# Optimization experiments

Hardware: AMD Instinct MI355X
Metric: run time of the kernel (lower is better)

Reference implementation:

```python
import jax, jax.numpy as jnp
import numpy as np

T = 0.2  # temperature (init default)
EPS = 1e-12  # torch F.normalize eps


def setup_inputs() -> dict:
    key = jax.random.key(0)
    k1, k2 = jax.random.split(key, 2)
    b, in_c, out_c = 8192, 128, 128
    anchor_features = jax.random.normal(k1, (b, in_c), dtype=jnp.float32)
    W = jax.random.normal(k2, (in_c, out_c), dtype=jnp.float32) * (1.0 / np.sqrt(in_c))
    bias = jnp.zeros((out_c,), dtype=jnp.float32)
    return {"anchor_features": anchor_features, "W": W, "bias": bias}


def reference(anchor_features, W, bias):
    # MappingLayer: linear projection + L2 normalize, then pairwise cosine sims.
    z = anchor_features @ W + bias                                  # [b, d]
    z = z / jnp.maximum(jnp.linalg.norm(z, axis=-1, keepdims=True), EPS)
    sim = (z @ z.T) / T                                             # [b, b]
    b = sim.shape[0]
    idx = jnp.arange(b)
    j0 = (idx + b // 2) % b                                         # positive pair index
    # Fused symmetric exp matrix: E[i,j] = exp(sim[i,j] + sim[j,i])
    E = jnp.exp(sim + sim.T)                                        # [b, b]
    top = E[idx, j0]                                                # exp(s_ij0 + s_j0i)
    bottom = jnp.sum(E, axis=1) - E[idx, idx]                       # sum over j != i
    loss = -jnp.sum(jnp.log(top / bottom)) / (b - 1)
    return loss
```

## Files before the change

kernel.cpp:

```cpp
#include <hip/hip_runtime.h>
#include <stdint.h>

typedef short bf16x8 __attribute__((ext_vector_type(8)));
typedef float f32x4 __attribute__((ext_vector_type(4)));

#define NROWS 8192
#define DIM   128
#define ZSCALE 3.7982824f
#define LN2F  0.6931471805599453f


__device__ __forceinline__ unsigned short f32_to_bf16_bits(float x) {
  union { float f; uint32_t u; } v; v.f = x;
  uint32_t r = v.u + 0x7FFFu + ((v.u >> 16) & 1u);
  return (unsigned short)(r >> 16);
}

__global__ __launch_bounds__(256) void k_wprep(const float* __restrict__ W,
                                               unsigned short* __restrict__ Wtf,
                                               float* __restrict__ sumexp,
                                               float* __restrict__ topacc) {
  const int idx = blockIdx.x * 256 + threadIdx.x;
  if (idx < 2048) {
    const int l = idx & 63, chunk = idx >> 6;
    const int tj = chunk >> 2, ks = chunk & 3, g = l >> 4, q = l & 15;
    const float* wp = W + (size_t)(ks * 32 + g * 8) * DIM + tj * 16 + q;
    bf16x8 o;
#pragma unroll
    for (int e = 0; e < 8; ++e) o[e] = (short)f32_to_bf16_bits(wp[(size_t)e * DIM]);
    *(bf16x8*)(Wtf + (size_t)idx * 8) = o;
  }
  if (idx < NROWS) sumexp[idx] = 0.f;
  if (idx == 0) topacc[0] = 0.f;
}

__global__ __launch_bounds__(256) void k_proj_norm(
    const float* __restrict__ anchor, const unsigned short* __restrict__ Wtf,
    const float* __restrict__ bias, unsigned short* __restrict__ zf) {
  __shared__ float part[4][16][132];
  const int t = threadIdx.x;
  const int wv = t >> 6, l = t & 63, g = l >> 4, q = l & 15;
  const int rb = blockIdx.x * 16;

  const float* ap = anchor + (size_t)(rb + q) * DIM + wv * 32 + g * 8;
  const f32x4 a0 = *(const f32x4*)ap, a1 = *(const f32x4*)(ap + 4);
  bf16x8 a;
#pragma unroll
  for (int e = 0; e < 4; ++e) {
    a[e] = (short)f32_to_bf16_bits(a0[e]);
    a[4 + e] = (short)f32_to_bf16_bits(a1[e]);
  }

  f32x4 acc[8];
#pragma unroll
  for (int tj = 0; tj < 8; ++tj) acc[tj] = (f32x4){0.f, 0.f, 0.f, 0.f};
#pragma unroll
  for (int tj = 0; tj < 8; ++tj) {
    const bf16x8 b = *(const bf16x8*)(Wtf + (size_t)((tj * 4 + wv) * 64 + l) * 8);
    acc[tj] = __builtin_amdgcn_mfma_f32_16x16x32_bf16(a, b, acc[tj], 0, 0, 0);
  }

#pragma unroll
  for (int tj = 0; tj < 8; ++tj)
#pragma unroll
    for (int r = 0; r < 4; ++r) part[wv][4 * g + r][tj * 16 + q] = acc[tj][r];
  __syncthreads();

  const int row = t >> 4, c = t & 15;
  float v[8];
#pragma unroll
  for (int e = 0; e < 8; ++e) v[e] = bias[c * 8 + e];
#pragma unroll
  for (int s = 0; s < 4; ++s) {
    const f32x4 p0 = *(const f32x4*)&part[s][row][c * 8];
    const f32x4 p1 = *(const f32x4*)&part[s][row][c * 8 + 4];
#pragma unroll
    for (int e = 0; e < 4; ++e) {
      v[e] += p0[e];
      v[4 + e] += p1[e];
    }
  }
  float ss = 0.f;
#pragma unroll
  for (int e = 0; e < 8; ++e) ss += v[e] * v[e];
#pragma unroll
  for (int m = 1; m < 16; m <<= 1) ss += __shfl_xor(ss, m, 64);
  const float inv = ZSCALE / fmaxf(sqrtf(ss), 1e-12f);

  bf16x8 o;
#pragma unroll
  for (int e = 0; e < 8; ++e) o[e] = (short)f32_to_bf16_bits(v[e] * inv);
  const int ks = c >> 2, gg = c & 3;
  *(bf16x8*)(zf + (size_t)(((blockIdx.x * 4 + ks) * 64) + gg * 16 + row) * 8) = o;
}

__global__ __launch_bounds__(256) void k_simloss(
    const unsigned short* __restrict__ zf, float* __restrict__ sumexp,
    float* __restrict__ topacc) {
  const int t = threadIdx.x;
  const int wv = t >> 6, l = t & 63, g = l >> 4, q = l & 15;
  const int igrp = (int)blockIdx.x >> 5, jbi = (int)blockIdx.x & 31;
  const int r0 = igrp * 256 + wv * 64;
  const int cb = jbi * 256;
  const int posr = (r0 + 4096) & 8191;

  bf16x8 afr[4][4];
#pragma unroll
  for (int ti = 0; ti < 4; ++ti)
#pragma unroll
    for (int ks = 0; ks < 4; ++ks)
      afr[ti][ks] = *(const bf16x8*)(
          zf + (size_t)((((r0 >> 4) + ti) * 4 + ks) * 512 + l * 8));

  float sums[4][4];
#pragma unroll
  for (int ti = 0; ti < 4; ++ti)
#pragma unroll
    for (int r = 0; r < 4; ++r) sums[ti][r] = 0.f;
  float topv = 0.f;

  bool qeq[4];
#pragma unroll
  for (int r = 0; r < 4; ++r) qeq[r] = (q == 4 * g + r);

  auto LOADB = [&](bf16x8 b[4], int c0) {
    const int bcol = c0 >> 4;
#pragma unroll
    for (int ks = 0; ks < 4; ++ks)
      b[ks] = *(const bf16x8*)(zf + (size_t)((bcol * 4 + ks) * 512 + l * 8));
  };
  auto COMPUTE = [&](const bf16x8 b[4], int c0) {
    f32x4 acc[4];
#pragma unroll
    for (int ti = 0; ti < 4; ++ti) acc[ti] = (f32x4){0.f, 0.f, 0.f, 0.f};
#pragma unroll
    for (int ti = 0; ti < 4; ++ti)
#pragma unroll
      for (int ks = 0; ks < 4; ++ks)
        acc[ti] = __builtin_amdgcn_mfma_f32_16x16x32_bf16(afr[ti][ks], b[ks],
                                                          acc[ti], 0, 0, 0);
    const int dgo = c0 - r0, pso = c0 - posr;
    const int dgti = ((unsigned)dgo < 64u) ? (dgo >> 4) : -1;
    const int psti = ((unsigned)pso < 64u) ? (pso >> 4) : -1;
#pragma unroll
    for (int ti = 0; ti < 4; ++ti) {
#pragma unroll
      for (int r = 0; r < 4; ++r) {
        const float d = acc[ti][r];
        float e = __builtin_amdgcn_exp2f(d);
        if (ti == dgti && qeq[r]) e = 0.f;
        if (ti == psti && qeq[r]) topv += d;
        sums[ti][r] += e;
      }
    }
  };

  bf16x8 bA[4], bB[4];
  LOADB(bA, cb);
#pragma unroll
  for (int p = 0; p < 8; ++p) {
    LOADB(bB, cb + p * 32 + 16);
    COMPUTE(bA, cb + p * 32);
    if (p < 7) LOADB(bA, cb + p * 32 + 32);
    COMPUTE(bB, cb + p * 32 + 16);
  }

#pragma unroll
  for (int ti = 0; ti < 4; ++ti)
#pragma unroll
    for (int r = 0; r < 4; ++r) {
#pragma unroll
      for (int m = 1; m < 16; m <<= 1)
        sums[ti][r] += __shfl_xor(sums[ti][r], m, 64);
    }
  if (q == 0) {
#pragma unroll
    for (int ti = 0; ti < 4; ++ti)
#pragma unroll
      for (int r = 0; r < 4; ++r)
        atomicAdd(&sumexp[r0 + ti * 16 + 4 * g + r], sums[ti][r]);
  }

  if ((posr & ~255) == cb) {
#pragma unroll
    for (int m = 1; m < 64; m <<= 1) topv += __shfl_xor(topv, m, 64);
    if (l == 0) atomicAdd(topacc, topv);
  }
}

__global__ __launch_bounds__(256) void k_final(const float* __restrict__ sumexp,
                                               const float* __restrict__ topacc,
                                               float* __restrict__ out) {
  __shared__ float red[4];
  const int t = threadIdx.x;
  float s = 0.f;
  for (int r = t; r < NROWS; r += 256) s += logf(sumexp[r]);
#pragma unroll
  for (int m = 1; m < 64; m <<= 1) s += __shfl_xor(s, m, 64);
  if ((t & 63) == 0) red[t >> 6] = s;
  __syncthreads();
  if (t == 0) {
    const float S1 = red[0] + red[1] + red[2] + red[3];
    out[0] = (S1 - LN2F * topacc[0]) * (1.0f / (float)(NROWS - 1));
  }
}

extern "C" void kernel_launch(void* const* d_in, const int* in_sizes, int n_in,
                              void* d_out, int out_size, void* d_ws, size_t ws_size,
                              hipStream_t stream) {
  const float* anchor = (const float*)d_in[0];
  const float* W = (const float*)d_in[1];
  const float* bias = (const float*)d_in[2];
  float* out = (float*)d_out;

  char* ws = (char*)d_ws;
  unsigned short* zf = (unsigned short*)ws;
  float* sumexp = (float*)(ws + (size_t)2 * 1024 * 1024);
  float* topacc = (float*)(ws + (size_t)2 * 1024 * 1024 + 32768);
  unsigned short* Wtf = (unsigned short*)(ws + (size_t)2 * 1024 * 1024 + 36864);

  k_wprep<<<dim3(64), dim3(256), 0, stream>>>(W, Wtf, sumexp, topacc);
  k_proj_norm<<<dim3(NROWS / 16), dim3(256), 0, stream>>>(anchor, Wtf, bias, zf);
  k_simloss<<<dim3(32 * 32), dim3(256), 0, stream>>>(zf, sumexp, topacc);
  k_final<<<dim3(1), dim3(256), 0, stream>>>(sumexp, topacc, out);
}
```

Measured before the change: 51.13 us.

## Exploit symmetry of sim matrix to compute only upper-triangular block tiles

Because the fused exp matrix is symmetric, the similarity kernel now launches only upper-triangular 256x256 block tiles (528 instead of 1024). Off-diagonal tiles add their exp values to both the row sums and, through per-column reductions and atomics, the column sums. The positive-pair term is counted once and doubled. The projection kernel also changes to a single wave per 16 rows doing the full K loop, so the cross-wave shared-memory reduction goes away, and the final reduction uses 1024 threads with log2. This roughly halves the MFMA and exp work, at the cost of extra column atomics and a triangular index decode.

Result: no change. 52.09 us (+1.9%).

```diff
diff --git a/kernel.cpp b/kernel.cpp
--- a/kernel.cpp
+++ b/kernel.cpp
@@ -34,64 +34,174 @@
   if (idx == 0) topacc[0] = 0.f;
 }
 
-__global__ __launch_bounds__(256) void k_proj_norm(
+__global__ __launch_bounds__(64) void k_proj_norm(
     const float* __restrict__ anchor, const unsigned short* __restrict__ Wtf,
     const float* __restrict__ bias, unsigned short* __restrict__ zf) {
-  __shared__ float part[4][16][132];
-  const int t = threadIdx.x;
-  const int wv = t >> 6, l = t & 63, g = l >> 4, q = l & 15;
+  __shared__ __align__(16) float part[16][132];
+  const int l = threadIdx.x, g = l >> 4, q = l & 15;
   const int rb = blockIdx.x * 16;
 
-  const float* ap = anchor + (size_t)(rb + q) * DIM + wv * 32 + g * 8;
-  const f32x4 a0 = *(const f32x4*)ap, a1 = *(const f32x4*)(ap + 4);
-  bf16x8 a;
-#pragma unroll
-  for (int e = 0; e < 4; ++e) {
-    a[e] = (short)f32_to_bf16_bits(a0[e]);
-    a[4 + e] = (short)f32_to_bf16_bits(a1[e]);
+  bf16x8 a[4];
+#pragma unroll
+  for (int ks = 0; ks < 4; ++ks) {
+    const float* ap = anchor + (size_t)(rb + q) * DIM + ks * 32 + g * 8;
+    const f32x4 a0 = *(const f32x4*)ap, a1 = *(const f32x4*)(ap + 4);
+#pragma unroll
+    for (int e = 0; e < 4; ++e) {
+      a[ks][e] = (short)f32_to_bf16_bits(a0[e]);
+      a[ks][4 + e] = (short)f32_to_bf16_bits(a1[e]);
+    }
   }
 
   f32x4 acc[8];
 #pragma unroll
   for (int tj = 0; tj < 8; ++tj) acc[tj] = (f32x4){0.f, 0.f, 0.f, 0.f};
 #pragma unroll
+  for (int tj = 0; tj < 8; ++tj)
+#pragma unroll
+    for (int ks = 0; ks < 4; ++ks) {
+      const bf16x8 b = *(const bf16x8*)(Wtf + (size_t)((tj * 4 + ks) * 64 + l) * 8);
+      acc[tj] = __builtin_amdgcn_mfma_f32_16x16x32_bf16(a[ks], b, acc[tj], 0, 0, 0);
+    }
+
+  float sumsq[4] = {0.f, 0.f, 0.f, 0.f};
+#pragma unroll
   for (int tj = 0; tj < 8; ++tj) {
-    const bf16x8 b = *(const bf16x8*)(Wtf + (size_t)((tj * 4 + wv) * 64 + l) * 8);
-    acc[tj] = __builtin_amdgcn_mfma_f32_16x16x32_bf16(a, b, acc[tj], 0, 0, 0);
-  }
+    const float bv = bias[tj * 16 + q];
+#pragma unroll
+    for (int r = 0; r < 4; ++r) {
+      acc[tj][r] += bv;
+      sumsq[r] += acc[tj][r] * acc[tj][r];
+    }
+  }
+#pragma unroll
+  for (int r = 0; r < 4; ++r) {
+#pragma unroll
+    for (int m = 1; m < 16; m <<= 1) sumsq[r] += __shfl_xor(sumsq[r], m, 64);
+  }
+  float inv[4];
+#pragma unroll
+  for (int r = 0; r < 4; ++r) inv[r] = ZSCALE / fmaxf(sqrtf(sumsq[r]), 1e-12f);
 
 #pragma unroll
   for (int tj = 0; tj < 8; ++tj)
 #pragma unroll
-    for (int r = 0; r < 4; ++r) part[wv][4 * g + r][tj * 16 + q] = acc[tj][r];
-  __syncthreads();
-
-  const int row = t >> 4, c = t & 15;
-  float v[8];
-#pragma unroll
-  for (int e = 0; e < 8; ++e) v[e] = bias[c * 8 + e];
-#pragma unroll
-  for (int s = 0; s < 4; ++s) {
-    const f32x4 p0 = *(const f32x4*)&part[s][row][c * 8];
-    const f32x4 p1 = *(const f32x4*)&part[s][row][c * 8 + 4];
+    for (int r = 0; r < 4; ++r) part[4 * g + r][tj * 16 + q] = acc[tj][r] * inv[r];
+
+#pragma unroll
+  for (int ks = 0; ks < 4; ++ks) {
+    const f32x4 p0 = *(const f32x4*)&part[q][ks * 32 + g * 8];
+    const f32x4 p1 = *(const f32x4*)&part[q][ks * 32 + g * 8 + 4];
+    bf16x8 o;
 #pragma unroll
     for (int e = 0; e < 4; ++e) {
-      v[e] += p0[e];
-      v[4 + e] += p1[e];
-    }
-  }
-  float ss = 0.f;
-#pragma unroll
-  for (int e = 0; e < 8; ++e) ss += v[e] * v[e];
-#pragma unroll
-  for (int m = 1; m < 16; m <<= 1) ss += __shfl_xor(ss, m, 64);
-  const float inv = ZSCALE / fmaxf(sqrtf(ss), 1e-12f);
-
-  bf16x8 o;
-#pragma unroll
-  for (int e = 0; e < 8; ++e) o[e] = (short)f32_to_bf16_bits(v[e] * inv);
-  const int ks = c >> 2, gg = c & 3;
-  *(bf16x8*)(zf + (size_t)(((blockIdx.x * 4 + ks) * 64) + gg * 16 + row) * 8) = o;
+      o[e] = (short)f32_to_bf16_bits(p0[e]);
+      o[4 + e] = (short)f32_to_bf16_bits(p1[e]);
+    }
+    *(bf16x8*)(zf + (size_t)((blockIdx.x * 4 + ks) * 64 + l) * 8) = o;
+  }
+}
+
+template <int MODE>
+__device__ __forceinline__ void simloss_body(
+    const unsigned short* __restrict__ zf, float* __restrict__ sumexp,
+    float* __restrict__ topacc, const int r0, const int cb, const int l,
+    const int g, const int q) {
+  bf16x8 afr[4][4];
+#pragma unroll
+  for (int ti = 0; ti < 4; ++ti)
+#pragma unroll
+    for (int ks = 0; ks < 4; ++ks)
+      afr[ti][ks] = *(const bf16x8*)(
+          zf + (size_t)((((r0 >> 4) + ti) * 4 + ks) * 512 + l * 8));
+
+  float sums[4][4];
+#pragma unroll
+  for (int ti = 0; ti < 4; ++ti)
+#pragma unroll
+    for (int r = 0; r < 4; ++r) sums[ti][r] = 0.f;
+  float topv = 0.f;
+  const int posr = r0 + 4096;
+
+  bool qeq[4];
+#pragma unroll
+  for (int r = 0; r < 4; ++r) qeq[r] = (q == 4 * g + r);
+
+  auto LOADB = [&](bf16x8 b[4], int c0) {
+    const int bcol = c0 >> 4;
+#pragma unroll
+    for (int ks = 0; ks < 4; ++ks)
+      b[ks] = *(const bf16x8*)(zf + (size_t)((bcol * 4 + ks) * 512 + l * 8));
+  };
+  auto COMPUTE = [&](const bf16x8 b[4], int c0) {
+    f32x4 acc[4];
+#pragma unroll
+    for (int ti = 0; ti < 4; ++ti) acc[ti] = (f32x4){0.f, 0.f, 0.f, 0.f};
+#pragma unroll
+    for (int ti = 0; ti < 4; ++ti)
+#pragma unroll
+      for (int ks = 0; ks < 4; ++ks)
+        acc[ti] = __builtin_amdgcn_mfma_f32_16x16x32_bf16(afr[ti][ks], b[ks],
+                                                          acc[ti], 0, 0, 0);
+    int dgti = -1, psti = -1;
+    if (MODE == 0) {
+      const int dgo = c0 - r0;
+      dgti = ((unsigned)dgo < 64u) ? (dgo >> 4) : -1;
+    }
+    if (MODE == 2) {
+      const int pso = c0 - posr;
+      psti = ((unsigned)pso < 64u) ? (pso >> 4) : -1;
+    }
+    float cs = 0.f;
+#pragma unroll
+    for (int ti = 0; ti < 4; ++ti)
+#pragma unroll
+      for (int r = 0; r < 4; ++r) {
+        const float d = acc[ti][r];
+        float e = __builtin_amdgcn_exp2f(d);
+        if (MODE == 0 && ti == dgti && qeq[r]) e = 0.f;
+        if (MODE == 2 && ti == psti && qeq[r]) topv += d;
+        sums[ti][r] += e;
+        if (MODE != 0) cs += e;
+      }
+    if (MODE != 0) {
+      cs += __shfl_xor(cs, 16, 64);
+      cs += __shfl_xor(cs, 32, 64);
+      if (l < 16) atomicAdd(&sumexp[c0 + q], cs);
+    }
+  };
+
+  bf16x8 bA[4], bB[4];
+  LOADB(bA, cb);
+#pragma unroll
+  for (int p = 0; p < 8; ++p) {
+    LOADB(bB, cb + p * 32 + 16);
+    COMPUTE(bA, cb + p * 32);
+    if (p < 7) LOADB(bA, cb + p * 32 + 32);
+    COMPUTE(bB, cb + p * 32 + 16);
+  }
+
+#pragma unroll
+  for (int ti = 0; ti < 4; ++ti)
+#pragma unroll
+    for (int r = 0; r < 4; ++r) {
+#pragma unroll
+      for (int m = 1; m < 16; m <<= 1)
+        sums[ti][r] += __shfl_xor(sums[ti][r], m, 64);
+    }
+  if (q == 0) {
+#pragma unroll
+    for (int ti = 0; ti < 4; ++ti)
+#pragma unroll
+      for (int r = 0; r < 4; ++r)
+        atomicAdd(&sumexp[r0 + ti * 16 + 4 * g + r], sums[ti][r]);
+  }
+
+  if (MODE == 2) {
+#pragma unroll
+    for (int m = 1; m < 64; m <<= 1) topv += __shfl_xor(topv, m, 64);
+    if (l == 0) atomicAdd(topacc, 2.f * topv);
+  }
 }
 
 __global__ __launch_bounds__(256) void k_simloss(
@@ -99,109 +209,32 @@
     float* __restrict__ topacc) {
   const int t = threadIdx.x;
   const int wv = t >> 6, l = t & 63, g = l >> 4, q = l & 15;
-  const int igrp = (int)blockIdx.x >> 5, jbi = (int)blockIdx.x & 31;
+  int rem = (int)blockIdx.x, igrp = 0;
+  while (rem >= 32 - igrp) { rem -= 32 - igrp; ++igrp; }
+  const int jbi = igrp + rem;
   const int r0 = igrp * 256 + wv * 64;
   const int cb = jbi * 256;
-  const int posr = (r0 + 4096) & 8191;
-
-  bf16x8 afr[4][4];
-#pragma unroll
-  for (int ti = 0; ti < 4; ++ti)
-#pragma unroll
-    for (int ks = 0; ks < 4; ++ks)
-      afr[ti][ks] = *(const bf16x8*)(
-          zf + (size_t)((((r0 >> 4) + ti) * 4 + ks) * 512 + l * 8));
-
-  float sums[4][4];
-#pragma unroll
-  for (int ti = 0; ti < 4; ++ti)
-#pragma unroll
-    for (int r = 0; r < 4; ++r) sums[ti][r] = 0.f;
-  float topv = 0.f;
-
-  bool qeq[4];
-#pragma unroll
-  for (int r = 0; r < 4; ++r) qeq[r] = (q == 4 * g + r);
-
-  auto LOADB = [&](bf16x8 b[4], int c0) {
-    const int bcol = c0 >> 4;
-#pragma unroll
-    for (int ks = 0; ks < 4; ++ks)
-      b[ks] = *(const bf16x8*)(zf + (size_t)((bcol * 4 + ks) * 512 + l * 8));
-  };
-  auto COMPUTE = [&](const bf16x8 b[4], int c0) {
-    f32x4 acc[4];
-#pragma unroll
-    for (int ti = 0; ti < 4; ++ti) acc[ti] = (f32x4){0.f, 0.f, 0.f, 0.f};
-#pragma unroll
-    for (int ti = 0; ti < 4; ++ti)
-#pragma unroll
-      for (int ks = 0; ks < 4; ++ks)
-        acc[ti] = __builtin_amdgcn_mfma_f32_16x16x32_bf16(afr[ti][ks], b[ks],
-                                                          acc[ti], 0, 0, 0);
-    const int dgo = c0 - r0, pso = c0 - posr;
-    const int dgti = ((unsigned)dgo < 64u) ? (dgo >> 4) : -1;
-    const int psti = ((unsigned)pso < 64u) ? (pso >> 4) : -1;
-#pragma unroll
-    for (int ti = 0; ti < 4; ++ti) {
-#pragma unroll
-      for (int r = 0; r < 4; ++r) {
-        const float d = acc[ti][r];
-        float e = __builtin_amdgcn_exp2f(d);
-        if (ti == dgti && qeq[r]) e = 0.f;
-        if (ti == psti && qeq[r]) topv += d;
-        sums[ti][r] += e;
-      }
-    }
-  };
-
-  bf16x8 bA[4], bB[4];
-  LOADB(bA, cb);
-#pragma unroll
-  for (int p = 0; p < 8; ++p) {
-    LOADB(bB, cb + p * 32 + 16);
-    COMPUTE(bA, cb + p * 32);
-    if (p < 7) LOADB(bA, cb + p * 32 + 32);
-    COMPUTE(bB, cb + p * 32 + 16);
-  }
-
-#pragma unroll
-  for (int ti = 0; ti < 4; ++ti)
-#pragma unroll
-    for (int r = 0; r < 4; ++r) {
-#pragma unroll
-      for (int m = 1; m < 16; m <<= 1)
-        sums[ti][r] += __shfl_xor(sums[ti][r], m, 64);
-    }
-  if (q == 0) {
-#pragma unroll
-    for (int ti = 0; ti < 4; ++ti)
-#pragma unroll
-      for (int r = 0; r < 4; ++r)
-        atomicAdd(&sumexp[r0 + ti * 16 + 4 * g + r], sums[ti][r]);
-  }
-
-  if ((posr & ~255) == cb) {
-#pragma unroll
-    for (int m = 1; m < 64; m <<= 1) topv += __shfl_xor(topv, m, 64);
-    if (l == 0) atomicAdd(topacc, topv);
-  }
-}
-
-__global__ __launch_bounds__(256) void k_final(const float* __restrict__ sumexp,
-                                               const float* __restrict__ topacc,
-                                               float* __restrict__ out) {
-  __shared__ float red[4];
+  if (igrp == jbi)           simloss_body<0>(zf, sumexp, topacc, r0, cb, l, g, q);
+  else if (jbi == igrp + 16) simloss_body<2>(zf, sumexp, topacc, r0, cb, l, g, q);
+  else                       simloss_body<1>(zf, sumexp, topacc, r0, cb, l, g, q);
+}
+
+__global__ __launch_bounds__(1024) void k_final(const float* __restrict__ sumexp,
+                                                const float* __restrict__ topacc,
+                                                float* __restrict__ out) {
+  __shared__ float red[16];
   const int t = threadIdx.x;
   float s = 0.f;
-  for (int r = t; r < NROWS; r += 256) s += logf(sumexp[r]);
+  for (int r = t; r < NROWS; r += 1024) s += __log2f(sumexp[r]);
 #pragma unroll
   for (int m = 1; m < 64; m <<= 1) s += __shfl_xor(s, m, 64);
   if ((t & 63) == 0) red[t >> 6] = s;
   __syncthreads();
   if (t == 0) {
-    const float S1 = red[0] + red[1] + red[2] + red[3];
-    out[0] = (S1 - LN2F * topacc[0]) * (1.0f / (float)(NROWS - 1));
+    float S1 = 0.f;
+#pragma unroll
+    for (int i = 0; i < 16; ++i) S1 += red[i];
+    out[0] = LN2F * (S1 - topacc[0]) * (1.0f / (float)(NROWS - 1));
   }
 }
 
@@ -220,7 +253,7 @@
   unsigned short* Wtf = (unsigned short*)(ws + (size_t)2 * 1024 * 1024 + 36864);
 
   k_wprep<<<dim3(64), dim3(256), 0, stream>>>(W, Wtf, sumexp, topacc);
-  k_proj_norm<<<dim3(NROWS / 16), dim3(256), 0, stream>>>(anchor, Wtf, bias, zf);
-  k_simloss<<<dim3(32 * 32), dim3(256), 0, stream>>>(zf, sumexp, topacc);
-  k_final<<<dim3(1), dim3(256), 0, stream>>>(sumexp, topacc, out);
-}
+  k_proj_norm<<<dim3(NROWS / 16), dim3(64), 0, stream>>>(anchor, Wtf, bias, zf);
+  k_simloss<<<dim3(528), dim3(256), 0, stream>>>(zf, sumexp, topacc);
+  k_final<<<dim3(1), dim3(1024), 0, stream>>>(sumexp, topacc, out);
+}
```

## Stage B tiles into LDS via async global_load_lds double buffering

Applied to the files above, without the earlier changes.

Before, each of the four waves loaded the shared column block of z straight from global memory into registers. Now the block stages each 64-column chunk into a double-buffered 32 KB LDS area using direct global-to-LDS loads, so each tile is fetched once per block and all waves read it from LDS. This adds a barrier per chunk and more LDS use, which may lower occupancy. The final reduction kernel also moves to 1024 threads and uses log2 with a single ln2 scale at the end.

Result: faster. 42.09 us (-17.7%).

```diff
diff --git a/kernel.cpp b/kernel.cpp
--- a/kernel.cpp
+++ b/kernel.cpp
@@ -15,6 +15,11 @@
   uint32_t r = v.u + 0x7FFFu + ((v.u >> 16) & 1u);
   return (unsigned short)(r >> 16);
 }
+
+#define GLOAD_LDS16(gsrc, ldst)                                      \
+  __builtin_amdgcn_global_load_lds(                                  \
+      (const __attribute__((address_space(1))) unsigned int*)(gsrc), \
+      (__attribute__((address_space(3))) unsigned int*)(ldst), 16, 0, 0)
 
 __global__ __launch_bounds__(256) void k_wprep(const float* __restrict__ W,
                                                unsigned short* __restrict__ Wtf,
@@ -97,6 +102,7 @@
 __global__ __launch_bounds__(256) void k_simloss(
     const unsigned short* __restrict__ zf, float* __restrict__ sumexp,
     float* __restrict__ topacc) {
+  __shared__ __align__(16) unsigned short lz[2 * 8192];
   const int t = threadIdx.x;
   const int wv = t >> 6, l = t & 63, g = l >> 4, q = l & 15;
   const int igrp = (int)blockIdx.x >> 5, jbi = (int)blockIdx.x & 31;
@@ -119,51 +125,57 @@
     for (int r = 0; r < 4; ++r) sums[ti][r] = 0.f;
   float topv = 0.f;
 
-  bool qeq[4];
-#pragma unroll
-  for (int r = 0; r < 4; ++r) qeq[r] = (q == 4 * g + r);
-
-  auto LOADB = [&](bf16x8 b[4], int c0) {
-    const int bcol = c0 >> 4;
-#pragma unroll
-    for (int ks = 0; ks < 4; ++ks)
-      b[ks] = *(const bf16x8*)(zf + (size_t)((bcol * 4 + ks) * 512 + l * 8));
-  };
-  auto COMPUTE = [&](const bf16x8 b[4], int c0) {
-    f32x4 acc[4];
-#pragma unroll
-    for (int ti = 0; ti < 4; ++ti) acc[ti] = (f32x4){0.f, 0.f, 0.f, 0.f};
-#pragma unroll
-    for (int ti = 0; ti < 4; ++ti)
+#define STAGE(bufsel, c_)                                                    \
+  _Pragma("unroll") for (int it = 0; it < 4; ++it) {                         \
+    const char* src = (const char*)zf +                                      \
+                      ((size_t)(jbi * 64 + (c_)*16) << 10) +                 \
+                      ((it * 256 + t) << 4);                                 \
+    GLOAD_LDS16(src, (char*)lz + (bufsel)*16384 + it * 4096 + wv * 1024);    \
+  }
+
+  STAGE(0, 0);
+  __syncthreads();
+
+#pragma unroll
+  for (int c = 0; c < 4; ++c) {
+    if (c < 3) STAGE((c + 1) & 1, c + 1);
+
+    const unsigned short* buf = lz + (c & 1) * 8192;
+#pragma unroll
+    for (int jt = 0; jt < 4; ++jt) {
+      bf16x8 bfr[4];
 #pragma unroll
       for (int ks = 0; ks < 4; ++ks)
-        acc[ti] = __builtin_amdgcn_mfma_f32_16x16x32_bf16(afr[ti][ks], b[ks],
-                                                          acc[ti], 0, 0, 0);
-    const int dgo = c0 - r0, pso = c0 - posr;
-    const int dgti = ((unsigned)dgo < 64u) ? (dgo >> 4) : -1;
-    const int psti = ((unsigned)pso < 64u) ? (pso >> 4) : -1;
-#pragma unroll
-    for (int ti = 0; ti < 4; ++ti) {
-#pragma unroll
-      for (int r = 0; r < 4; ++r) {
-        const float d = acc[ti][r];
-        float e = __builtin_amdgcn_exp2f(d);
-        if (ti == dgti && qeq[r]) e = 0.f;
-        if (ti == psti && qeq[r]) topv += d;
-        sums[ti][r] += e;
-      }
+        bfr[ks] = *(const bf16x8*)(buf + (size_t)((jt * 4 + ks) * 64 + l) * 8);
+
+      f32x4 acc[4];
+#pragma unroll
+      for (int ti = 0; ti < 4; ++ti) acc[ti] = (f32x4){0.f, 0.f, 0.f, 0.f};
+#pragma unroll
+      for (int ti = 0; ti < 4; ++ti)
+#pragma unroll
+        for (int ks = 0; ks < 4; ++ks)
+          acc[ti] = __builtin_amdgcn_mfma_f32_16x16x32_bf16(afr[ti][ks], bfr[ks],
+                                                            acc[ti], 0, 0, 0);
+
+      const int c0 = cb + c * 64 + jt * 16;
+      const int dgo = c0 - r0, pso = c0 - posr;
+      const int dgti = ((unsigned)dgo < 64u) ? (dgo >> 4) : -1;
+      const int psti = ((unsigned)pso < 64u) ? (pso >> 4) : -1;
+#pragma unroll
+      for (int ti = 0; ti < 4; ++ti)
+#pragma unroll
+        for (int r = 0; r < 4; ++r) {
+          const float d = acc[ti][r];
+          float e = __builtin_amdgcn_exp2f(d);
+          if (ti == dgti && q == 4 * g + r) e = 0.f;
+          if (ti == psti && q == 4 * g + r) topv += d;
+          sums[ti][r] += e;
+        }
     }
-  };
-
-  bf16x8 bA[4], bB[4];
-  LOADB(bA, cb);
-#pragma unroll
-  for (int p = 0; p < 8; ++p) {
-    LOADB(bB, cb + p * 32 + 16);
-    COMPUTE(bA, cb + p * 32);
-    if (p < 7) LOADB(bA, cb + p * 32 + 32);
-    COMPUTE(bB, cb + p * 32 + 16);
-  }
+    __syncthreads();
+  }
+#undef STAGE
 
 #pragma unroll
   for (int ti = 0; ti < 4; ++ti)
@@ -188,20 +200,22 @@
   }
 }
 
-__global__ __launch_bounds__(256) void k_final(const float* __restrict__ sumexp,
-                                               const float* __restrict__ topacc,
-                                               float* __restrict__ out) {
-  __shared__ float red[4];
+__global__ __launch_bounds__(1024) void k_final(const float* __restrict__ sumexp,
+                                                const float* __restrict__ topacc,
+                                                float* __restrict__ out) {
+  __shared__ float red[16];
   const int t = threadIdx.x;
   float s = 0.f;
-  for (int r = t; r < NROWS; r += 256) s += logf(sumexp[r]);
+  for (int r = t; r < NROWS; r += 1024) s += __log2f(sumexp[r]);
 #pragma unroll
   for (int m = 1; m < 64; m <<= 1) s += __shfl_xor(s, m, 64);
   if ((t & 63) == 0) red[t >> 6] = s;
   __syncthreads();
   if (t == 0) {
-    const float S1 = red[0] + red[1] + red[2] + red[3];
-    out[0] = (S1 - LN2F * topacc[0]) * (1.0f / (float)(NROWS - 1));
+    float S1 = 0.f;
+#pragma unroll
+    for (int i = 0; i < 16; ++i) S1 += red[i];
+    out[0] = LN2F * (S1 - topacc[0]) * (1.0f / (float)(NROWS - 1));
   }
 }
 
@@ -222,5 +236,5 @@
   k_wprep<<<dim3(64), dim3(256), 0, stream>>>(W, Wtf, sumexp, topacc);
   k_proj_norm<<<dim3(NROWS / 16), dim3(256), 0, stream>>>(anchor, Wtf, bias, zf);
   k_simloss<<<dim3(32 * 32), dim3(256), 0, stream>>>(zf, sumexp, topacc);
-  k_final<<<dim3(1), dim3(256), 0, stream>>>(sumexp, topacc, out);
-}
+  k_final<<<dim3(1), dim3(1024), 0, stream>>>(sumexp, topacc, out);
+}
```
